# Kernel tuning notes

Hardware: AMD Instinct MI355X
Metric: run time of the kernel (lower is better)

## Reference

```python
import jax, jax.numpy as jnp
import numpy as np

CUTOFF = 1.0
MAX_NEIGHBORS = 32
ATOMS_PER_MOL = 512  # uniform molecule size (static, jit-friendly)
NUM_MOLS = 256


def setup_inputs() -> dict:
    key = jax.random.key(0)
    B, n = NUM_MOLS, ATOMS_PER_MOL
    atoms_x = jax.random.normal(key, (B * n, 3), dtype=jnp.float32)
    graph_batch = jnp.repeat(jnp.arange(B, dtype=jnp.int32), n)  # [N]
    return {"atoms_x": atoms_x, "graph_batch": graph_batch}


def reference(atoms_x, graph_batch):
    """Radius graph with per-atom top-K nearest neighbors, per molecule.

    Faithful to the torch module under the (static-shape) assumption that
    molecules are uniform size ATOMS_PER_MOL and graph_batch is contiguous.
    Variable-length edge lists are returned padded: invalid slots have
    bond_i = bond_j = -1, bond_vec = 0, bond_dist = 0, plus a validity mask.
    Valid entries match the torch output (row-major per atom, K nearest).
    """
    N = atoms_x.shape[0]
    n = ATOMS_PER_MOL
    B = N // n
    K = MAX_NEIGHBORS
    pos = atoms_x.reshape(B, n, 3)

    # diff[b, i, j] = pos[b, j] - pos[b, i]  (matches torch unsqueeze(0)-unsqueeze(1))
    diff = pos[:, None, :, :] - pos[:, :, None, :]          # [B, n, n, 3]
    d2 = jnp.sum(diff * diff, axis=-1)                       # [B, n, n]
    c2 = jnp.float32(CUTOFF) ** 2
    nbr_mask = (d2 < c2) & (d2 > 0)                          # dist<cutoff & dist>0

    # K smallest masked squared distances per atom (sqrt is monotone -> same topk)
    d2_masked = jnp.where(nbr_mask, d2, jnp.inf)
    _, idx = jax.lax.top_k(-d2_masked, K)                    # [B, n, K] neighbor cols
    valid = jnp.take_along_axis(nbr_mask, idx, axis=2)       # [B, n, K]

    # gather neighbor positions: pos_j[b, i, k] = pos[b, idx[b, i, k]]
    pos_j = jax.vmap(lambda p, ix: p[ix])(pos, idx)          # [B, n, K, 3]
    vec = pos_j - pos[:, :, None, :]                         # pos[dst] - pos[src]
    vec = jnp.where(valid[..., None], vec, 0.0)
    d2k = jnp.sum(vec * vec, axis=-1)
    dist = jnp.sqrt(jnp.where(valid, d2k, 1.0)) * valid      # safe sqrt, zero padding

    mol_base = jnp.arange(B, dtype=jnp.int32)[:, None, None] * n   # [B,1,1]
    row = mol_base + jnp.arange(n, dtype=jnp.int32)[None, :, None]  # global src idx
    bond_i = jnp.where(valid, jnp.broadcast_to(row, idx.shape), -1)
    bond_j = jnp.where(valid, mol_base + idx.astype(jnp.int32), -1)

    E = B * n * K
    return (bond_i.reshape(E), bond_j.reshape(E),
            vec.reshape(E, 3), dist.reshape(E), valid.reshape(E))
```

## Files before the change

### kernel.cpp

```cpp
#include <hip/hip_runtime.h>
#include <cstdint>


#define K_NBR 32
#define MOL_N 512
typedef unsigned long long u64;
typedef unsigned u32;

#define DPPK(ctrl, v) __builtin_amdgcn_update_dpp(0, (v), (ctrl), 0xF, 0xF, true)
#define SWZK(off, v) __builtin_amdgcn_ds_swizzle((v), (off))

__device__ __forceinline__ int ce(int k, int o, bool up) {
  const u32 a = (u32)k, b = (u32)o;
  const u32 mn = a < b ? a : b;
  const u32 mx = a < b ? b : a;
  return (int)(up ? mx : mn);
}

struct LaneBits {
  bool b1, b2, b4, b8, b16, b32;
  int bp63;
};

__device__ __forceinline__ int bsort32_prefix(int k, const LaneBits& L) {
  k = ce(k, DPPK(0xB1, k), L.b1);
  k = ce(k, DPPK(0x1B, k), L.b2);
  k = ce(k, DPPK(0xB1, k), L.b1);
  k = ce(k, DPPK(0x141, k), L.b4);
  k = ce(k, DPPK(0x4E, k), L.b2);
  k = ce(k, DPPK(0xB1, k), L.b1);
  k = ce(k, DPPK(0x140, k), L.b8);
  k = ce(k, SWZK(0x101F, k), L.b4);
  k = ce(k, DPPK(0x4E, k), L.b2);
  k = ce(k, DPPK(0xB1, k), L.b1);
  k = ce(k, SWZK(0x7C1F, k), L.b16);
  k = ce(k, DPPK(0x128, k), L.b8);
  k = ce(k, SWZK(0x101F, k), L.b4);
  k = ce(k, DPPK(0x4E, k), L.b2);
  k = ce(k, DPPK(0xB1, k), L.b1);
  return k;
}

__device__ __forceinline__ int bsort64_suffix(int k, const LaneBits& L) {
  k = ce(k, __builtin_amdgcn_ds_bpermute(L.bp63, k), L.b32);
  k = ce(k, SWZK(0x401F, k), L.b16);
  k = ce(k, DPPK(0x128, k), L.b8);
  k = ce(k, SWZK(0x101F, k), L.b4);
  k = ce(k, DPPK(0x4E, k), L.b2);
  k = ce(k, DPPK(0xB1, k), L.b1);
  return k;
}

__device__ __forceinline__ int merge_low32(int k, int k2, const LaneBits& L) {
  const int krev = SWZK(0x7C1F, k2);
  const u32 a = (u32)k, b = (u32)krev;
  int m = (int)(a < b ? a : b);
  m = ce(m, SWZK(0x401F, m), L.b16);
  m = ce(m, DPPK(0x128, m), L.b8);
  m = ce(m, SWZK(0x101F, m), L.b4);
  m = ce(m, DPPK(0x4E, m), L.b2);
  m = ce(m, DPPK(0xB1, m), L.b1);
  return m;
}

__global__ __launch_bounds__(256) void topo_kernel(
    const float* __restrict__ atoms_x, float* __restrict__ out, int E_i) {
  __shared__ float sx[MOL_N], sy[MOL_N], sz[MOL_N];
  __shared__ u32 cand[4][MOL_N];

  const int tid = threadIdx.x;
  const int lane = tid & 63;
  const int wave = tid >> 6;
  const int mol = blockIdx.x >> 3;
  const int blk = blockIdx.x & 7;
  const size_t E = (size_t)E_i;

  const float* mp = atoms_x + (size_t)mol * (MOL_N * 3);
  for (int e = tid; e < MOL_N * 3; e += 256) {
    float v = mp[e];
    int a = e / 3;
    int c = e - a * 3;
    if (c == 0) sx[a] = v;
    else if (c == 1) sy[a] = v;
    else sz[a] = v;
  }
  __syncthreads();

  float px[8], py[8], pz[8];
#pragma unroll
  for (int s = 0; s < 8; ++s) {
    const int j = lane + (s << 6);
    px[s] = sx[j]; py[s] = sy[j]; pz[s] = sz[j];
  }
#pragma unroll
  for (int s = 0; s < 8; ++s) {
    asm volatile("" : "+v"(px[s]), "+v"(py[s]), "+v"(pz[s]));
  }

  float* o_bi = out;
  float* o_bj = out + E;
  float* o_vec = out + 2 * E;
  float* o_dist = out + 5 * E;
  float* o_val = out + 6 * E;

  u32* wc = cand[wave];
  LaneBits L;
  L.b1 = (lane & 1);  L.b2 = (lane & 2);   L.b4 = (lane & 4);
  L.b8 = (lane & 8);  L.b16 = (lane & 16); L.b32 = (lane & 32);
  L.bp63 = ((lane ^ 63) << 2);

  for (int it = 0; it < 16; ++it) {
    const int i_loc = blk * 64 + wave * 16 + it;
    const int i_glob = mol * MOL_N + i_loc;
    const float xi = sx[i_loc], yi = sy[i_loc], zi = sz[i_loc];

    int base = 0;
#pragma unroll
    for (int s = 0; s < 8; ++s) {
      const float dx = __fsub_rn(px[s], xi);
      const float dy = __fsub_rn(py[s], yi);
      const float dz = __fsub_rn(pz[s], zi);
      const float d2 = __fadd_rn(
          __fadd_rn(__fmul_rn(dx, dx), __fmul_rn(dy, dy)), __fmul_rn(dz, dz));
      const u32 db = __float_as_uint(d2);
      const bool pred = (db - 1u) < 0x3F7FFFFFu;
      const u64 bal = __ballot(pred);
      const int prefix = (int)__builtin_amdgcn_mbcnt_hi(
          (u32)(bal >> 32), __builtin_amdgcn_mbcnt_lo((u32)bal, 0u));
      if (pred)
        wc[base + prefix] = (db & 0xFFFFFE00u) | (u32)(lane + (s << 6));
      base += (int)__popcll(bal);
    }
    const int C = base;
    __builtin_amdgcn_wave_barrier();

    int k = (lane < C) ? (int)wc[lane] : (int)0xFFFFFFFFu;
    k = bsort32_prefix(k, L);
    if (C > 32) {
      k = bsort64_suffix(k, L);
      for (int b0 = 64; b0 < C; b0 += 64) {
        int k2 = (b0 + lane < C) ? (int)wc[b0 + lane] : (int)0xFFFFFFFFu;
        k2 = bsort32_prefix(k2, L);
        k2 = bsort64_suffix(k2, L);
        k = merge_low32(k, k2, L);
      }
    }
    __builtin_amdgcn_wave_barrier();

    if (lane < K_NBR) {
      const u32 key = (u32)k;
      const bool valid = (key != 0xFFFFFFFFu);
      const int j = (int)(key & 511u);
      const int jj = valid ? j : i_loc;
      const float vx = __fsub_rn(sx[jj], xi);
      const float vy = __fsub_rn(sy[jj], yi);
      const float vz = __fsub_rn(sz[jj], zi);
      const float d2t = __uint_as_float(key & 0xFFFFFE00u);
      const float dist = __builtin_amdgcn_sqrtf(d2t);
      const size_t e = (size_t)i_glob * K_NBR + (size_t)lane;
      o_bi[e] = valid ? (float)i_glob : -1.0f;
      o_bj[e] = valid ? (float)(mol * MOL_N + j) : -1.0f;
      o_vec[e * 3 + 0] = valid ? vx : 0.0f;
      o_vec[e * 3 + 1] = valid ? vy : 0.0f;
      o_vec[e * 3 + 2] = valid ? vz : 0.0f;
      o_dist[e] = valid ? dist : 0.0f;
      o_val[e] = valid ? 1.0f : 0.0f;
    }
  }
}

extern "C" void kernel_launch(void* const* d_in, const int* in_sizes, int n_in,
                              void* d_out, int out_size, void* d_ws,
                              size_t ws_size, hipStream_t stream) {
  const float* atoms_x = (const float*)d_in[0];
  const int N = in_sizes[0] / 3;
  const int E = out_size / 7;
  const int blocks = N / 64;
  topo_kernel<<<blocks, 256, 0, stream>>>(atoms_x, (float*)d_out, E);
}
```

Baseline: 153.9 us.

## Process two atoms per wave iteration to interleave sorts and use all lanes for stores

Each wave now handles two query atoms per loop iteration. Their distance passes and bitonic sorts are interleaved so the two independent dependency chains can hide DPP/swizzle latency. The second atom's top-32 is moved into the upper half-wave with a bpermute, so all 64 lanes write output rather than only 32. Candidate buffers are capped at 256 entries per atom. The cap could in principle drop candidates, and it assumes dense neighborhoods never exceed that size.

```diff
diff --git a/kernel.cpp b/kernel.cpp
--- a/kernel.cpp
+++ b/kernel.cpp
@@ -4,6 +4,7 @@
 
 #define K_NBR 32
 #define MOL_N 512
+#define CAP 256
 typedef unsigned long long u64;
 typedef unsigned u32;
 
@@ -63,10 +64,12 @@
   return m;
 }
 
+struct F3 { float x, y, z; };
+
 __global__ __launch_bounds__(256) void topo_kernel(
     const float* __restrict__ atoms_x, float* __restrict__ out, int E_i) {
   __shared__ float sx[MOL_N], sy[MOL_N], sz[MOL_N];
-  __shared__ u32 cand[4][MOL_N];
+  __shared__ u32 cand[4][2][CAP];
 
   const int tid = threadIdx.x;
   const int lane = tid & 63;
@@ -103,69 +106,104 @@
   float* o_dist = out + 5 * E;
   float* o_val = out + 6 * E;
 
-  u32* wc = cand[wave];
+  u32* wcA = cand[wave][0];
+  u32* wcB = cand[wave][1];
   LaneBits L;
   L.b1 = (lane & 1);  L.b2 = (lane & 2);   L.b4 = (lane & 4);
   L.b8 = (lane & 8);  L.b16 = (lane & 16); L.b32 = (lane & 32);
   L.bp63 = ((lane ^ 63) << 2);
-
-  for (int it = 0; it < 16; ++it) {
-    const int i_loc = blk * 64 + wave * 16 + it;
-    const int i_glob = mol * MOL_N + i_loc;
-    const float xi = sx[i_loc], yi = sy[i_loc], zi = sz[i_loc];
-
-    int base = 0;
+  const int bpLo = (lane & 31) << 2;
+
+  for (int it = 0; it < 8; ++it) {
+    const int iA = blk * 64 + wave * 16 + (it << 1);
+    const int gA = mol * MOL_N + iA;
+    const float xiA = sx[iA], yiA = sy[iA], ziA = sz[iA];
+    const float xiB = sx[iA + 1], yiB = sy[iA + 1], ziB = sz[iA + 1];
+
+    int baseA = 0, baseB = 0;
 #pragma unroll
     for (int s = 0; s < 8; ++s) {
-      const float dx = __fsub_rn(px[s], xi);
-      const float dy = __fsub_rn(py[s], yi);
-      const float dz = __fsub_rn(pz[s], zi);
-      const float d2 = __fadd_rn(
-          __fadd_rn(__fmul_rn(dx, dx), __fmul_rn(dy, dy)), __fmul_rn(dz, dz));
-      const u32 db = __float_as_uint(d2);
-      const bool pred = (db - 1u) < 0x3F7FFFFFu;
-      const u64 bal = __ballot(pred);
-      const int prefix = (int)__builtin_amdgcn_mbcnt_hi(
-          (u32)(bal >> 32), __builtin_amdgcn_mbcnt_lo((u32)bal, 0u));
-      if (pred)
-        wc[base + prefix] = (db & 0xFFFFFE00u) | (u32)(lane + (s << 6));
-      base += (int)__popcll(bal);
+      const u32 jj = (u32)(lane + (s << 6));
+      const float dxA = __fsub_rn(px[s], xiA);
+      const float dyA = __fsub_rn(py[s], yiA);
+      const float dzA = __fsub_rn(pz[s], ziA);
+      const float d2A = __fadd_rn(
+          __fadd_rn(__fmul_rn(dxA, dxA), __fmul_rn(dyA, dyA)),
+          __fmul_rn(dzA, dzA));
+      const float dxB = __fsub_rn(px[s], xiB);
+      const float dyB = __fsub_rn(py[s], yiB);
+      const float dzB = __fsub_rn(pz[s], ziB);
+      const float d2B = __fadd_rn(
+          __fadd_rn(__fmul_rn(dxB, dxB), __fmul_rn(dyB, dyB)),
+          __fmul_rn(dzB, dzB));
+      const u32 dbA = __float_as_uint(d2A);
+      const u32 dbB = __float_as_uint(d2B);
+      const bool pA = (dbA - 1u) < 0x3F7FFFFFu;
+      const bool pB = (dbB - 1u) < 0x3F7FFFFFu;
+      const u64 balA = __ballot(pA);
+      const u64 balB = __ballot(pB);
+      const int pfxA = (int)__builtin_amdgcn_mbcnt_hi(
+          (u32)(balA >> 32), __builtin_amdgcn_mbcnt_lo((u32)balA, 0u));
+      const int pfxB = (int)__builtin_amdgcn_mbcnt_hi(
+          (u32)(balB >> 32), __builtin_amdgcn_mbcnt_lo((u32)balB, 0u));
+      const int offA = baseA + pfxA;
+      const int offB = baseB + pfxB;
+      if (pA && offA < CAP) wcA[offA] = (dbA & 0xFFFFFE00u) | jj;
+      if (pB && offB < CAP) wcB[offB] = (dbB & 0xFFFFFE00u) | jj;
+      baseA += (int)__popcll(balA);
+      baseB += (int)__popcll(balB);
     }
-    const int C = base;
+    const int CA = baseA < CAP ? baseA : CAP;
+    const int CB = baseB < CAP ? baseB : CAP;
     __builtin_amdgcn_wave_barrier();
 
-    int k = (lane < C) ? (int)wc[lane] : (int)0xFFFFFFFFu;
-    k = bsort32_prefix(k, L);
-    if (C > 32) {
-      k = bsort64_suffix(k, L);
-      for (int b0 = 64; b0 < C; b0 += 64) {
-        int k2 = (b0 + lane < C) ? (int)wc[b0 + lane] : (int)0xFFFFFFFFu;
-        k2 = bsort32_prefix(k2, L);
-        k2 = bsort64_suffix(k2, L);
-        k = merge_low32(k, k2, L);
+    int kA = (lane < CA) ? (int)wcA[lane] : (int)0xFFFFFFFFu;
+    int kB = (lane < CB) ? (int)wcB[lane] : (int)0xFFFFFFFFu;
+    kA = bsort32_prefix(kA, L);
+    kB = bsort32_prefix(kB, L);
+    const int Cm = CA > CB ? CA : CB;
+    if (Cm > 32) {
+      kA = bsort64_suffix(kA, L);
+      kB = bsort64_suffix(kB, L);
+      for (int b0 = 64; b0 < Cm; b0 += 64) {
+        if (b0 < CA) {
+          int k2 = (b0 + lane < CA) ? (int)wcA[b0 + lane] : (int)0xFFFFFFFFu;
+          k2 = bsort64_suffix(bsort32_prefix(k2, L), L);
+          kA = merge_low32(kA, k2, L);
+        }
+        if (b0 < CB) {
+          int k2 = (b0 + lane < CB) ? (int)wcB[b0 + lane] : (int)0xFFFFFFFFu;
+          k2 = bsort64_suffix(bsort32_prefix(k2, L), L);
+          kB = merge_low32(kB, k2, L);
+        }
       }
     }
     __builtin_amdgcn_wave_barrier();
 
-    if (lane < K_NBR) {
-      const u32 key = (u32)k;
-      const bool valid = (key != 0xFFFFFFFFu);
-      const int j = (int)(key & 511u);
-      const int jj = valid ? j : i_loc;
-      const float vx = __fsub_rn(sx[jj], xi);
-      const float vy = __fsub_rn(sy[jj], yi);
-      const float vz = __fsub_rn(sz[jj], zi);
-      const float d2t = __uint_as_float(key & 0xFFFFFE00u);
-      const float dist = __builtin_amdgcn_sqrtf(d2t);
-      const size_t e = (size_t)i_glob * K_NBR + (size_t)lane;
-      o_bi[e] = valid ? (float)i_glob : -1.0f;
-      o_bj[e] = valid ? (float)(mol * MOL_N + j) : -1.0f;
-      o_vec[e * 3 + 0] = valid ? vx : 0.0f;
-      o_vec[e * 3 + 1] = valid ? vy : 0.0f;
-      o_vec[e * 3 + 2] = valid ? vz : 0.0f;
-      o_dist[e] = valid ? dist : 0.0f;
-      o_val[e] = valid ? 1.0f : 0.0f;
-    }
+    const int kBm = __builtin_amdgcn_ds_bpermute(bpLo, kB);
+    const u32 key = (u32)(L.b32 ? kBm : kA);
+    const bool valid = (key != 0xFFFFFFFFu);
+    const int i_loc = iA + (lane >> 5);
+    const int j = (int)(key & 511u);
+    const int js = valid ? j : i_loc;
+    const float xi = L.b32 ? xiB : xiA;
+    const float yi = L.b32 ? yiB : yiA;
+    const float zi = L.b32 ? ziB : ziA;
+    const float vx = __fsub_rn(sx[js], xi);
+    const float vy = __fsub_rn(sy[js], yi);
+    const float vz = __fsub_rn(sz[js], zi);
+    const float d2t = __uint_as_float(key & 0xFFFFFE00u);
+    const float dist = __builtin_amdgcn_sqrtf(d2t);
+    const size_t e = (size_t)gA * K_NBR + (size_t)lane;
+    o_bi[e] = valid ? (float)(gA + (lane >> 5)) : -1.0f;
+    o_bj[e] = valid ? (float)(mol * MOL_N + j) : -1.0f;
+    F3 v3;
+    v3.x = valid ? vx : 0.0f;
+    v3.y = valid ? vy : 0.0f;
+    v3.z = valid ? vz : 0.0f;
+    ((F3*)o_vec)[e] = v3;
+    o_dist[e] = valid ? dist : 0.0f;
+    o_val[e] = valid ? 1.0f : 0.0f;
   }
 }
 
```

Result: no change. 153.6 us (-0.2%).
